# Kernel optimization log

Hardware: AMD Instinct MI355X
Metric: run time of the kernel (lower is better)

Reference implementation:

```python
import jax, jax.numpy as jnp
import numpy as np

DEPTH = 12
EMB = 768
HEADS = 12
HEAD_DIM = EMB // HEADS
FF = 4 * EMB
EPS = 1e-6
SCALE = HEAD_DIM ** -0.5


def _layernorm(x, w, b):
    mu = jnp.mean(x, axis=-1, keepdims=True)
    var = jnp.mean(jnp.square(x - mu), axis=-1, keepdims=True)
    return (x - mu) * jax.lax.rsqrt(var + EPS) * w + b


def setup_inputs() -> dict:
    key = jax.random.key(0)
    ks = jax.random.split(key, 13)
    s = 0.02
    d = {
        "x": jax.random.normal(ks[0], (8, 1024, EMB), dtype=jnp.float32),
        "ln1_w": jnp.ones((DEPTH, EMB), jnp.float32),
        "ln1_b": jnp.zeros((DEPTH, EMB), jnp.float32),
        "qkv_w": jax.random.normal(ks[1], (DEPTH, EMB, 3 * EMB), jnp.float32) * s,
        "qkv_b": jnp.zeros((DEPTH, 3 * EMB), jnp.float32),
        "proj_w": jax.random.normal(ks[2], (DEPTH, EMB, EMB), jnp.float32) * s,
        "proj_b": jnp.zeros((DEPTH, EMB), jnp.float32),
        "ln2_w": jnp.ones((DEPTH, EMB), jnp.float32),
        "ln2_b": jnp.zeros((DEPTH, EMB), jnp.float32),
        "fc1_w": jax.random.normal(ks[3], (DEPTH, EMB, FF), jnp.float32) * s,
        "fc1_b": jnp.zeros((DEPTH, FF), jnp.float32),
        "fc2_w": jax.random.normal(ks[4], (DEPTH, FF, EMB), jnp.float32) * s,
        "fc2_b": jnp.zeros((DEPTH, EMB), jnp.float32),
    }
    return d


def _block(x, p):
    (l1w, l1b, qw, qb, pw, pb, l2w, l2b, f1w, f1b, f2w, f2b) = p
    B, N, C = x.shape
    # --- attention sub-block (pre-LN, residual add) ---
    h = _layernorm(x, l1w, l1b)
    qkv = (h @ qw + qb).reshape(B, N, 3, HEADS, HEAD_DIM)
    qkv = jnp.transpose(qkv, (2, 0, 3, 1, 4))  # [3,B,H,N,D]
    q, k, v = qkv[0], qkv[1], qkv[2]
    att = jnp.einsum('bhqd,bhkd->bhqk', q, k) * SCALE
    att = jax.nn.softmax(att, axis=-1)
    out = jnp.einsum('bhqk,bhkd->bhqd', att, v)
    out = jnp.transpose(out, (0, 2, 1, 3)).reshape(B, N, C)
    x = x + (out @ pw + pb)
    # --- feed-forward sub-block ---
    h = _layernorm(x, l2w, l2b)
    h = jax.nn.gelu(h @ f1w + f1b, approximate=False)  # nn.GELU default = exact
    x = x + (h @ f2w + f2b)
    return x, None


def reference(x, ln1_w, ln1_b, qkv_w, qkv_b, proj_w, proj_b,
              ln2_w, ln2_b, fc1_w, fc1_b, fc2_w, fc2_b):
    params = (ln1_w, ln1_b, qkv_w, qkv_b, proj_w, proj_b,
              ln2_w, ln2_b, fc1_w, fc1_b, fc2_w, fc2_b)
    out, _ = jax.lax.scan(_block, x, params)
    return out
```

## Files before the change

kernel.cpp:

```cpp
#include <hip/hip_runtime.h>
#include <cstdint>
#include <cstddef>

#define NLAYER 12
#define EMB 768
#define NH 12
#define HD 64
#define FF 3072
#define SEQ 1024
#define BATCH 8
#define NTOK (BATCH * SEQ)

typedef unsigned short ushort_t;
typedef __attribute__((ext_vector_type(8))) short short8;
typedef __attribute__((ext_vector_type(4))) float floatx4;

typedef __attribute__((address_space(1))) void GV;
typedef __attribute__((address_space(3))) void LV;

__device__ __forceinline__ void async16(const void* g, void* l) {
  __builtin_amdgcn_global_load_lds((GV*)g, (LV*)l, 16, 0, 0);
}

__device__ __forceinline__ ushort_t f2bf(float f) {
  union { float f; unsigned u; } a; a.f = f;
  unsigned u = a.u;
  return (ushort_t)((u + 0x7fffu + ((u >> 16) & 1u)) >> 16);
}

__global__ __launch_bounds__(256) void kw_transpose(const float* __restrict__ src,
                                                    ushort_t* __restrict__ dst,
                                                    int K, int N) {
  size_t ls = (size_t)K * N;
  src += (size_t)blockIdx.z * ls;
  dst += (size_t)blockIdx.z * ls;
  int n0 = blockIdx.x * 64, k0 = blockIdx.y * 64;
  __shared__ ushort_t t[64][72];
  int tid = threadIdx.x;
  int r = tid >> 2, c0 = (tid & 3) * 16;
  const float* s = src + (size_t)(k0 + r) * N + n0 + c0;
#pragma unroll
  for (int j = 0; j < 16; j += 4) {
    float4 v = *(const float4*)(s + j);
    t[r][c0 + j + 0] = f2bf(v.x);
    t[r][c0 + j + 1] = f2bf(v.y);
    t[r][c0 + j + 2] = f2bf(v.z);
    t[r][c0 + j + 3] = f2bf(v.w);
  }
  __syncthreads();
  int n = tid >> 2;
  int kk0 = (tid & 3) * 16;
  ushort_t* d = dst + (size_t)(n0 + n) * K + k0 + kk0;
#pragma unroll
  for (int j = 0; j < 16; j += 8) {
    alignas(16) ushort_t tmp[8];
#pragma unroll
    for (int jj = 0; jj < 8; ++jj) tmp[jj] = t[kk0 + j + jj][n];
    *(uint4*)(d + j) = *(const uint4*)tmp;
  }
}

__global__ __launch_bounds__(256) void ln_kernel(const float* __restrict__ x,
                                                 const float* __restrict__ w,
                                                 const float* __restrict__ b,
                                                 ushort_t* __restrict__ out) {
  int wv = threadIdx.x >> 6, lane = threadIdx.x & 63;
  int row = blockIdx.x * 4 + wv;
  const float* xr = x + (size_t)row * EMB;
  float4 v[3];
  float s = 0.f, s2 = 0.f;
#pragma unroll
  for (int k = 0; k < 3; ++k) {
    v[k] = *(const float4*)(xr + lane * 4 + k * 256);
    s += v[k].x + v[k].y + v[k].z + v[k].w;
    s2 += v[k].x * v[k].x + v[k].y * v[k].y + v[k].z * v[k].z + v[k].w * v[k].w;
  }
#pragma unroll
  for (int off = 32; off > 0; off >>= 1) {
    s += __shfl_xor(s, off, 64);
    s2 += __shfl_xor(s2, off, 64);
  }
  float mu = s * (1.f / EMB);
  float var = s2 * (1.f / EMB) - mu * mu;
  float inv = rsqrtf(var + 1e-6f);
  ushort_t* orow = out + (size_t)row * EMB;
#pragma unroll
  for (int k = 0; k < 3; ++k) {
    int c = lane * 4 + k * 256;
    float4 wv4 = *(const float4*)(w + c);
    float4 bv4 = *(const float4*)(b + c);
    alignas(8) ushort_t t4[4];
    t4[0] = f2bf((v[k].x - mu) * inv * wv4.x + bv4.x);
    t4[1] = f2bf((v[k].y - mu) * inv * wv4.y + bv4.y);
    t4[2] = f2bf((v[k].z - mu) * inv * wv4.z + bv4.z);
    t4[3] = f2bf((v[k].w - mu) * inv * wv4.w + bv4.w);
    *(uint2*)(orow + c) = *(const uint2*)t4;
  }
}

__global__ __launch_bounds__(256) void v_transpose(const ushort_t* __restrict__ V,
                                                   ushort_t* __restrict__ Vt) {
  int bh = blockIdx.y, n0 = blockIdx.x * 64;
  const ushort_t* src = V + ((size_t)bh * SEQ + n0) * HD;
  ushort_t* dst = Vt + (size_t)bh * HD * SEQ;
  __shared__ ushort_t t[64][72];
  int tid = threadIdx.x;
#pragma unroll
  for (int i = 0; i < 2; ++i) {
    int c = tid + i * 256;
    int n = c >> 3, doff = (c & 7) * 8;
    *(uint4*)&t[n][doff] = *(const uint4*)(src + (size_t)n * HD + doff);
  }
  __syncthreads();
#pragma unroll
  for (int i = 0; i < 2; ++i) {
    int c = tid + i * 256;
    int d = c >> 3, noff = (c & 7) * 8;
    alignas(16) ushort_t tmp[8];
#pragma unroll
    for (int j = 0; j < 8; ++j) tmp[j] = t[noff + j][d];
    *(uint4*)(dst + (size_t)d * SEQ + n0 + noff) = *(const uint4*)tmp;
  }
}

template <int MODE, int TN>
__global__ __launch_bounds__(256) void gemm_kernel(
    const ushort_t* __restrict__ A, const ushort_t* __restrict__ Bt,
    int K, int N, const float* __restrict__ bias,
    const float* __restrict__ resid, float* __restrict__ outf,
    ushort_t* __restrict__ outb,
    ushort_t* __restrict__ qo, ushort_t* __restrict__ ko, ushort_t* __restrict__ vo) {
  constexpr int MT = (TN == 128) ? 4 : 2;
  constexpr int AELE = 128 * 32;
  constexpr int BELE = TN * 32;
  constexpr int BUFELE = AELE + BELE;
  __shared__ alignas(16) ushort_t smem[2 * BUFELE];

  int tid = threadIdx.x;
  int wv = tid >> 6, lane = tid & 63;
  int lm = lane & 15, lq = lane >> 4;
  int wm = (TN == 128) ? (wv >> 1) : wv;
  int wn = (TN == 128) ? (wv & 1) : 0;

  int Gx = gridDim.x;
  int hw = blockIdx.y * Gx + blockIdx.x;
  int xcd = hw & 7;
  int j = hw >> 3;
  int jq = j / Gx;
  int by = xcd + (jq << 3);
  int bx = j - jq * Gx;
  int m0 = by * 128, n0 = bx * TN;

  const ushort_t* Abase = A + (size_t)m0 * K;
  const ushort_t* Bbase = Bt + (size_t)n0 * K;

  auto stage = [&](int buf, int kt) {
    ushort_t* dA = smem + buf * BUFELE;
    ushort_t* dB = dA + AELE;
    int kOff = kt * 32;
#pragma unroll
    for (int i = 0; i < 2; ++i) {
      int c = wv * 64 + i * 256 + lane;
      int row = c >> 2, off = (c & 3) * 8;
      async16(Abase + (size_t)row * K + kOff + off, dA + (wv * 64 + i * 256) * 8);
    }
    if (TN == 128) {
#pragma unroll
      for (int i = 0; i < 2; ++i) {
        int c = wv * 64 + i * 256 + lane;
        int row = c >> 2, off = (c & 3) * 8;
        async16(Bbase + (size_t)row * K + kOff + off, dB + (wv * 64 + i * 256) * 8);
      }
    } else {
      int c = wv * 64 + lane;
      int row = c >> 2, off = (c & 3) * 8;
      async16(Bbase + (size_t)row * K + kOff + off, dB + (wv * 64) * 8);
    }
  };

  floatx4 acc[MT][4] = {};
  int kIters = K >> 5;

  stage(0, 0);
  __syncthreads();

  for (int kt = 0; kt < kIters; ++kt) {
    int cur = kt & 1;
    if (kt + 1 < kIters) stage(cur ^ 1, kt + 1);
    const ushort_t* sA = smem + cur * BUFELE;
    const ushort_t* sB = sA + AELE;
    short8 aF[MT], bF[4];
#pragma unroll
    for (int mt = 0; mt < MT; ++mt)
      aF[mt] = *(const short8*)(sA + (wm * (16 * MT) + mt * 16 + lm) * 32 + lq * 8);
#pragma unroll
    for (int nt = 0; nt < 4; ++nt)
      bF[nt] = *(const short8*)(sB + (wn * 64 + nt * 16 + lm) * 32 + lq * 8);
#pragma unroll
    for (int mt = 0; mt < MT; ++mt)
#pragma unroll
      for (int nt = 0; nt < 4; ++nt)
        acc[mt][nt] = __builtin_amdgcn_mfma_f32_16x16x32_bf16(aF[mt], bF[nt], acc[mt][nt], 0, 0, 0);
    __syncthreads();
  }

  float* sE = (float*)smem;
  float* eW = sE + wv * (16 * 68);
#pragma unroll
  for (int mt = 0; mt < MT; ++mt) {
#pragma unroll
    for (int nt = 0; nt < 4; ++nt)
#pragma unroll
      for (int r = 0; r < 4; ++r)
        eW[(lq * 4 + r) * 68 + nt * 16 + lm] = acc[mt][nt][r];
    __syncthreads();
    int gm_base = m0 + wm * (16 * MT) + mt * 16;
#pragma unroll
    for (int p = 0; p < 4; ++p) {
      int r16 = p * 4 + lq;
      int gm = gm_base + r16;
      int cc = lm * 4;
      int gn = n0 + wn * 64 + cc;
      float4 vv = *(float4*)(eW + r16 * 68 + cc);
      float4 bb = *(const float4*)(bias + gn);
      if (MODE == 1) {
        float4 rr = *(const float4*)(resid + (size_t)gm * N + gn);
        vv.x += bb.x + rr.x; vv.y += bb.y + rr.y;
        vv.z += bb.z + rr.z; vv.w += bb.w + rr.w;
        *(float4*)(outf + (size_t)gm * N + gn) = vv;
      } else if (MODE == 2) {
        float g0 = vv.x + bb.x, g1 = vv.y + bb.y, g2 = vv.z + bb.z, g3 = vv.w + bb.w;
        alignas(8) ushort_t t4[4];
        t4[0] = f2bf(0.5f * g0 * (1.f + erff(g0 * 0.70710678118654752f)));
        t4[1] = f2bf(0.5f * g1 * (1.f + erff(g1 * 0.70710678118654752f)));
        t4[2] = f2bf(0.5f * g2 * (1.f + erff(g2 * 0.70710678118654752f)));
        t4[3] = f2bf(0.5f * g3 * (1.f + erff(g3 * 0.70710678118654752f)));
        *(uint2*)(outb + (size_t)gm * N + gn) = *(const uint2*)t4;
      } else {
        int which = gn / 768;
        int rem = gn - which * 768;
        int h = rem >> 6, dd = rem & 63;
        float sc = (which == 0) ? 0.125f * 1.44269504088896341f : 1.0f;
        ushort_t* base = (which == 0) ? qo : (which == 1) ? ko : vo;
        int bidx = gm >> 10, nn = gm & 1023;
        alignas(8) ushort_t t4[4];
        t4[0] = f2bf((vv.x + bb.x) * sc);
        t4[1] = f2bf((vv.y + bb.y) * sc);
        t4[2] = f2bf((vv.z + bb.z) * sc);
        t4[3] = f2bf((vv.w + bb.w) * sc);
        *(uint2*)(base + ((size_t)((bidx * NH + h) * SEQ + nn)) * HD + dd) = *(const uint2*)t4;
      }
    }
    __syncthreads();
  }
}

__global__ __launch_bounds__(256, 3) void attn_kernel(const ushort_t* __restrict__ Q,
                                                      const ushort_t* __restrict__ Kin,
                                                      const ushort_t* __restrict__ Vt,
                                                      ushort_t* __restrict__ O) {
  __shared__ ushort_t sK[2 * 64 * 32];
  __shared__ ushort_t sV[2][2 * 64 * 32];
  __shared__ ushort_t sP[4 * 32 * 72];

  int flat = blockIdx.x;
  int xcd = flat & 7, idx = flat >> 3;
  int bh = ((idx >> 3) << 3) + xcd;
  int qb = idx & 7;

  int tid = threadIdx.x, wv = tid >> 6, lane = tid & 63;
  int lm = lane & 15, lq = lane >> 4;

  const ushort_t* Qp = Q + ((size_t)bh * SEQ + qb * 128 + wv * 32) * HD;
  const ushort_t* Kp = Kin + (size_t)bh * SEQ * HD;
  const ushort_t* Vp = Vt + (size_t)bh * HD * SEQ;

  short8 qF[2][2];
#pragma unroll
  for (int mi = 0; mi < 2; ++mi)
#pragma unroll
    for (int kd = 0; kd < 2; ++kd)
      qF[mi][kd] = *(const short8*)(Qp + (size_t)(mi * 16 + lm) * HD + kd * 32 + lq * 8);

#pragma unroll
  for (int i = 0; i < 2; ++i) {
    int s = i * 256 + wv * 64 + lane;
    int kd = s >> 8, row = (s >> 2) & 63, q = s & 3;
    async16(Kp + (size_t)row * HD + kd * 32 + q * 8, sK + (i * 256 + wv * 64) * 8);
  }
#pragma unroll
  for (int i = 0; i < 2; ++i) {
    int s = i * 256 + wv * 64 + lane;
    int ks = s >> 8, d = (s >> 2) & 63, q = s & 3;
    async16(Vp + (size_t)d * SEQ + ks * 32 + q * 8, sV[0] + (i * 256 + wv * 64) * 8);
  }
  __syncthreads();

  floatx4 oF[2][4] = {};
  float mrow[2][4], lrow[2][4];
#pragma unroll
  for (int mi = 0; mi < 2; ++mi)
#pragma unroll
    for (int r = 0; r < 4; ++r) { mrow[mi][r] = -1e30f; lrow[mi][r] = 0.f; }
  ushort_t* Pw = sP + wv * (32 * 72);

  for (int kt = 0; kt < SEQ / 64; ++kt) {
    const ushort_t* sVc = sV[kt & 1];
    floatx4 sF[2][4];
#pragma unroll
    for (int mi = 0; mi < 2; ++mi)
#pragma unroll
      for (int nt = 0; nt < 4; ++nt) sF[mi][nt] = floatx4{0.f, 0.f, 0.f, 0.f};
#pragma unroll
    for (int nt = 0; nt < 4; ++nt) {
      short8 kF0 = *(const short8*)(sK + (0 * 64 + nt * 16 + lm) * 32 + lq * 8);
      short8 kF1 = *(const short8*)(sK + (1 * 64 + nt * 16 + lm) * 32 + lq * 8);
#pragma unroll
      for (int mi = 0; mi < 2; ++mi) {
        sF[mi][nt] = __builtin_amdgcn_mfma_f32_16x16x32_bf16(qF[mi][0], kF0, sF[mi][nt], 0, 0, 0);
        sF[mi][nt] = __builtin_amdgcn_mfma_f32_16x16x32_bf16(qF[mi][1], kF1, sF[mi][nt], 0, 0, 0);
      }
    }
    __syncthreads();

    int nk = (kt < SEQ / 64 - 1) ? kt + 1 : kt;
    ushort_t* sVn = sV[(kt + 1) & 1];
#pragma unroll
    for (int i = 0; i < 2; ++i) {
      int s = i * 256 + wv * 64 + lane;
      int kd = s >> 8, row = (s >> 2) & 63, q = s & 3;
      async16(Kp + (size_t)(nk * 64 + row) * HD + kd * 32 + q * 8, sK + (i * 256 + wv * 64) * 8);
    }
#pragma unroll
    for (int i = 0; i < 2; ++i) {
      int s = i * 256 + wv * 64 + lane;
      int ks = s >> 8, d = (s >> 2) & 63, q = s & 3;
      async16(Vp + (size_t)d * SEQ + nk * 64 + ks * 32 + q * 8, sVn + (i * 256 + wv * 64) * 8);
    }

#pragma unroll
    for (int mi = 0; mi < 2; ++mi) {
#pragma unroll
      for (int r = 0; r < 4; ++r) {
        float mx = fmaxf(fmaxf(sF[mi][0][r], sF[mi][1][r]), fmaxf(sF[mi][2][r], sF[mi][3][r]));
#pragma unroll
        for (int off = 1; off < 16; off <<= 1) mx = fmaxf(mx, __shfl_xor(mx, off, 64));
        float mnew = fmaxf(mrow[mi][r], mx);
        float alpha = __builtin_amdgcn_exp2f(mrow[mi][r] - mnew);
        mrow[mi][r] = mnew;
        float rs = 0.f;
        int prow = (mi * 16 + lq * 4 + r) * 72;
#pragma unroll
        for (int nt = 0; nt < 4; ++nt) {
          float p = __builtin_amdgcn_exp2f(sF[mi][nt][r] - mnew);
          rs += p;
          Pw[prow + nt * 16 + lm] = f2bf(p);
        }
        lrow[mi][r] = lrow[mi][r] * alpha + rs;
#pragma unroll
        for (int dt = 0; dt < 4; ++dt) oF[mi][dt][r] *= alpha;
      }
    }

#pragma unroll
    for (int ks = 0; ks < 2; ++ks) {
      short8 pF[2];
#pragma unroll
      for (int mi = 0; mi < 2; ++mi)
        pF[mi] = *(const short8*)(Pw + (mi * 16 + lm) * 72 + ks * 32 + lq * 8);
#pragma unroll
      for (int dt = 0; dt < 4; ++dt) {
        short8 vF = *(const short8*)(sVc + (ks * 64 + dt * 16 + lm) * 32 + lq * 8);
#pragma unroll
        for (int mi = 0; mi < 2; ++mi)
          oF[mi][dt] = __builtin_amdgcn_mfma_f32_16x16x32_bf16(pF[mi], vF, oF[mi][dt], 0, 0, 0);
      }
    }
    __syncthreads();
  }

#pragma unroll
  for (int mi = 0; mi < 2; ++mi)
#pragma unroll
    for (int r = 0; r < 4; ++r)
#pragma unroll
      for (int off = 1; off < 16; off <<= 1)
        lrow[mi][r] += __shfl_xor(lrow[mi][r], off, 64);

  int b = bh / NH, h = bh - b * NH;
#pragma unroll
  for (int mi = 0; mi < 2; ++mi) {
#pragma unroll
    for (int r = 0; r < 4; ++r) {
      float invl = 1.0f / lrow[mi][r];
      int t = b * SEQ + qb * 128 + wv * 32 + mi * 16 + lq * 4 + r;
      ushort_t* orow = O + (size_t)t * EMB + h * HD;
#pragma unroll
      for (int dt = 0; dt < 4; ++dt) orow[dt * 16 + lm] = f2bf(oF[mi][dt][r] * invl);
    }
  }
}

extern "C" void kernel_launch(void* const* d_in, const int* in_sizes, int n_in,
                              void* d_out, int out_size, void* d_ws, size_t ws_size,
                              hipStream_t stream) {
  const float* xin = (const float*)d_in[0];
  const float* ln1_w = (const float*)d_in[1];
  const float* ln1_b = (const float*)d_in[2];
  const float* qkv_w = (const float*)d_in[3];
  const float* qkv_b = (const float*)d_in[4];
  const float* proj_w = (const float*)d_in[5];
  const float* proj_b = (const float*)d_in[6];
  const float* ln2_w = (const float*)d_in[7];
  const float* ln2_b = (const float*)d_in[8];
  const float* fc1_w = (const float*)d_in[9];
  const float* fc1_b = (const float*)d_in[10];
  const float* fc2_w = (const float*)d_in[11];
  const float* fc2_b = (const float*)d_in[12];

  size_t off = 0;
  char* ws = (char*)d_ws;
  auto alloc = [&](size_t bytes) -> void* {
    void* p = ws + off;
    off += (bytes + 255) & ~(size_t)255;
    return p;
  };
  ushort_t* wt_qkv = (ushort_t*)alloc((size_t)NLAYER * 2304 * 768 * 2);
  ushort_t* wt_proj = (ushort_t*)alloc((size_t)NLAYER * 768 * 768 * 2);
  ushort_t* wt_fc1 = (ushort_t*)alloc((size_t)NLAYER * 3072 * 768 * 2);
  ushort_t* wt_fc2 = (ushort_t*)alloc((size_t)NLAYER * 768 * 3072 * 2);
  float* X = (float*)alloc((size_t)NTOK * EMB * 4);
  ushort_t* Hb = (ushort_t*)alloc((size_t)NTOK * EMB * 2);
  ushort_t* Qb = (ushort_t*)alloc((size_t)NTOK * EMB * 2 * 4);
  ushort_t* Kb = Qb + (size_t)NTOK * EMB;
  ushort_t* Vb = Kb + (size_t)NTOK * EMB;
  ushort_t* Vtb = Vb + (size_t)NTOK * EMB;
  ushort_t* G = Qb;
  ushort_t* AO = (ushort_t*)alloc((size_t)NTOK * EMB * 2);

  hipMemcpyAsync(X, xin, (size_t)NTOK * EMB * 4, hipMemcpyDeviceToDevice, stream);

  dim3 b256(256);
  kw_transpose<<<dim3(36, 12, NLAYER), b256, 0, stream>>>(qkv_w, wt_qkv, 768, 2304);
  kw_transpose<<<dim3(12, 12, NLAYER), b256, 0, stream>>>(proj_w, wt_proj, 768, 768);
  kw_transpose<<<dim3(48, 12, NLAYER), b256, 0, stream>>>(fc1_w, wt_fc1, 768, 3072);
  kw_transpose<<<dim3(12, 48, NLAYER), b256, 0, stream>>>(fc2_w, wt_fc2, 3072, 768);

  for (int l = 0; l < NLAYER; ++l) {
    ln_kernel<<<NTOK / 4, b256, 0, stream>>>(X, ln1_w + l * 768, ln1_b + l * 768, Hb);
    gemm_kernel<0, 128><<<dim3(18, 64), b256, 0, stream>>>(
        Hb, wt_qkv + (size_t)l * 2304 * 768, 768, 2304, qkv_b + l * 2304,
        nullptr, nullptr, nullptr, Qb, Kb, Vb);
    v_transpose<<<dim3(16, 96), b256, 0, stream>>>(Vb, Vtb);
    attn_kernel<<<768, b256, 0, stream>>>(Qb, Kb, Vtb, AO);
    gemm_kernel<1, 64><<<dim3(12, 64), b256, 0, stream>>>(
        AO, wt_proj + (size_t)l * 768 * 768, 768, 768, proj_b + l * 768,
        X, X, nullptr, nullptr, nullptr, nullptr);
    ln_kernel<<<NTOK / 4, b256, 0, stream>>>(X, ln2_w + l * 768, ln2_b + l * 768, Hb);
    gemm_kernel<2, 128><<<dim3(24, 64), b256, 0, stream>>>(
        Hb, wt_fc1 + (size_t)l * 768 * 3072, 768, 3072, fc1_b + l * 3072,
        nullptr, nullptr, G, nullptr, nullptr, nullptr);
    float* outPtr = (l == NLAYER - 1) ? (float*)d_out : X;
    gemm_kernel<1, 64><<<dim3(12, 64), b256, 0, stream>>>(
        G, wt_fc2 + (size_t)l * 3072 * 768, 3072, 768, fc2_b + l * 768,
        X, outPtr, nullptr, nullptr, nullptr, nullptr);
  }
}
```

Measured before the change: 3.834 ms.

## Deepen GEMM async-load pipeline with multi-stage buffers, BK=64 and swizzled LDS

Replaces the GEMM's double-buffered K loop with a deeper pipeline: three stages for the TN=128 variant, and a K tile of 64 with XOR-swizzled LDS layout for the TN=64 variant. It waits on vmcnt counters instead of full __syncthreads, reads fragments into registers, then refills the freed buffer before issuing MFMAs. The aim is to hide global-to-LDS latency and cut bank conflicts and barrier stalls. It costs more LDS per block, which may lower occupancy, and the hand-counted vmcnt values must match the number of outstanding loads.

```diff
diff --git a/kernel.cpp b/kernel.cpp
--- a/kernel.cpp
+++ b/kernel.cpp
@@ -131,10 +131,17 @@
     ushort_t* __restrict__ outb,
     ushort_t* __restrict__ qo, ushort_t* __restrict__ ko, ushort_t* __restrict__ vo) {
   constexpr int MT = (TN == 128) ? 4 : 2;
-  constexpr int AELE = 128 * 32;
-  constexpr int BELE = TN * 32;
+  constexpr int BK = (TN == 64) ? 64 : 32;
+  constexpr int KD = BK / 32;
+  constexpr int NSTG = (TN == 64) ? 2 : 3;
+  constexpr int CPR = BK / 8;
+  constexpr int AELE = 128 * BK;
+  constexpr int BELE = TN * BK;
   constexpr int BUFELE = AELE + BELE;
-  __shared__ alignas(16) ushort_t smem[2 * BUFELE];
+  constexpr int AI = BK / 16;
+  constexpr int BI = (TN * BK) / 2048;
+  constexpr bool SWZ = (BK == 64);
+  __shared__ alignas(16) ushort_t smem[NSTG * BUFELE];
 
   int tid = threadIdx.x;
   int wv = tid >> 6, lane = tid & 63;
@@ -157,52 +164,81 @@
   auto stage = [&](int buf, int kt) {
     ushort_t* dA = smem + buf * BUFELE;
     ushort_t* dB = dA + AELE;
-    int kOff = kt * 32;
-#pragma unroll
-    for (int i = 0; i < 2; ++i) {
-      int c = wv * 64 + i * 256 + lane;
-      int row = c >> 2, off = (c & 3) * 8;
-      async16(Abase + (size_t)row * K + kOff + off, dA + (wv * 64 + i * 256) * 8);
-    }
-    if (TN == 128) {
-#pragma unroll
-      for (int i = 0; i < 2; ++i) {
-        int c = wv * 64 + i * 256 + lane;
-        int row = c >> 2, off = (c & 3) * 8;
-        async16(Bbase + (size_t)row * K + kOff + off, dB + (wv * 64 + i * 256) * 8);
-      }
+    int kOff = kt * BK;
+#pragma unroll
+    for (int i = 0; i < AI; ++i) {
+      int c = i * 256 + wv * 64 + lane;
+      int r = c / CPR, d = c % CPR;
+      int g = SWZ ? (d ^ (r & 7)) : d;
+      async16(Abase + (size_t)r * K + kOff + g * 8, dA + (i * 256 + wv * 64) * 8);
+    }
+#pragma unroll
+    for (int i = 0; i < BI; ++i) {
+      int c = i * 256 + wv * 64 + lane;
+      int r = c / CPR, d = c % CPR;
+      int g = SWZ ? (d ^ (r & 7)) : d;
+      async16(Bbase + (size_t)r * K + kOff + g * 8, dB + (i * 256 + wv * 64) * 8);
+    }
+  };
+
+  floatx4 acc[MT][4] = {};
+  int kIters = K / BK;
+
+  stage(0, 0);
+  stage(1, 1);
+  if constexpr (NSTG == 3) stage(2, 2);
+
+  for (int kt = 0; kt < kIters; ++kt) {
+    if constexpr (NSTG == 3) {
+      if (kt < kIters - 2)       asm volatile("s_waitcnt vmcnt(8)" ::: "memory");
+      else if (kt == kIters - 2) asm volatile("s_waitcnt vmcnt(4)" ::: "memory");
+      else                       asm volatile("s_waitcnt vmcnt(0)" ::: "memory");
     } else {
-      int c = wv * 64 + lane;
-      int row = c >> 2, off = (c & 3) * 8;
-      async16(Bbase + (size_t)row * K + kOff + off, dB + (wv * 64) * 8);
-    }
-  };
-
-  floatx4 acc[MT][4] = {};
-  int kIters = K >> 5;
-
-  stage(0, 0);
-  __syncthreads();
-
-  for (int kt = 0; kt < kIters; ++kt) {
-    int cur = kt & 1;
-    if (kt + 1 < kIters) stage(cur ^ 1, kt + 1);
+      if (kt < kIters - 1) asm volatile("s_waitcnt vmcnt(6)" ::: "memory");
+      else                 asm volatile("s_waitcnt vmcnt(0)" ::: "memory");
+    }
+    __builtin_amdgcn_s_barrier();
+
+    int cur = kt % NSTG;
     const ushort_t* sA = smem + cur * BUFELE;
     const ushort_t* sB = sA + AELE;
-    short8 aF[MT], bF[4];
-#pragma unroll
-    for (int mt = 0; mt < MT; ++mt)
-      aF[mt] = *(const short8*)(sA + (wm * (16 * MT) + mt * 16 + lm) * 32 + lq * 8);
-#pragma unroll
-    for (int nt = 0; nt < 4; ++nt)
-      bF[nt] = *(const short8*)(sB + (wn * 64 + nt * 16 + lm) * 32 + lq * 8);
-#pragma unroll
-    for (int mt = 0; mt < MT; ++mt)
-#pragma unroll
-      for (int nt = 0; nt < 4; ++nt)
-        acc[mt][nt] = __builtin_amdgcn_mfma_f32_16x16x32_bf16(aF[mt], bF[nt], acc[mt][nt], 0, 0, 0);
-    __syncthreads();
-  }
+    short8 aF[MT][KD], bF[4][KD];
+#pragma unroll
+    for (int mt = 0; mt < MT; ++mt) {
+      int row = wm * (16 * MT) + mt * 16 + lm;
+#pragma unroll
+      for (int kd = 0; kd < KD; ++kd) {
+        int ch = kd * 4 + lq;
+        if (SWZ) ch ^= (row & 7);
+        aF[mt][kd] = *(const short8*)(sA + row * BK + ch * 8);
+      }
+    }
+#pragma unroll
+    for (int nt = 0; nt < 4; ++nt) {
+      int row = wn * 64 + nt * 16 + lm;
+#pragma unroll
+      for (int kd = 0; kd < KD; ++kd) {
+        int ch = kd * 4 + lq;
+        if (SWZ) ch ^= (row & 7);
+        bF[nt][kd] = *(const short8*)(sB + row * BK + ch * 8);
+      }
+    }
+    asm volatile("s_waitcnt lgkmcnt(0)" ::: "memory");
+    __builtin_amdgcn_sched_barrier(0);
+    __builtin_amdgcn_s_barrier();
+
+    if (kt + NSTG < kIters) stage(cur, kt + NSTG);
+    __builtin_amdgcn_sched_barrier(0);
+
+#pragma unroll
+    for (int kd = 0; kd < KD; ++kd)
+#pragma unroll
+      for (int mt = 0; mt < MT; ++mt)
+#pragma unroll
+        for (int nt = 0; nt < 4; ++nt)
+          acc[mt][nt] = __builtin_amdgcn_mfma_f32_16x16x32_bf16(aF[mt][kd], bF[nt][kd], acc[mt][nt], 0, 0, 0);
+  }
+  __syncthreads();
 
   float* sE = (float*)smem;
   float* eW = sE + wv * (16 * 68);
```

Result: faster. 3.471 ms (-9.5%).
